# Performance work log

Measured on AMD Instinct MI355X. Metric: run time of the kernel, lower is better.

## Reference

```python
import jax, jax.numpy as jnp
import numpy as np

B = 256
IN_CH = 1
E = 8          # embedding_channels (power of 2)
DEPTH = 3      # log2(E)
T = 8192       # time_range
WINDOW = 2.0
K = 15         # kernel_size (odd -> torch 'same' == lax 'SAME')
TPI = 2.0 * np.pi


def conv1d(x, w, b, dilation=1, groups=1):
    # x: (B, Cin, T), w: (Cout, Cin/groups, K), b: (Cout,)
    out = jax.lax.conv_general_dilated(
        x, w, window_strides=(1,), padding='SAME',
        rhs_dilation=(dilation,),
        dimension_numbers=('NCH', 'OIH', 'NCH'),
        feature_group_count=groups)
    return out + b[None, :, None]


def setup_inputs() -> dict:
    key = jax.random.key(0)
    ks = jax.random.split(key, 14)
    s = 0.05
    x = jax.random.normal(ks[0], (B, T), jnp.float32)
    W1 = jax.random.normal(ks[1], (E, 2, 1, K), jnp.float32) * s   # per-channel Conv1d(1,2)
    b1 = jax.random.normal(ks[2], (E, 2), jnp.float32) * s
    W2 = jax.random.normal(ks[3], (E, 1, 2, K), jnp.float32) * s   # per-channel Conv1d(2,1)
    b2 = jax.random.normal(ks[4], (E, 1), jnp.float32) * s
    fcW = jax.random.normal(ks[5], (E, 2, T), jnp.float32) * 0.01  # per-channel Linear(T, 2)
    fcb = jax.random.normal(ks[6], (E, 2), jnp.float32) * s
    # deconv tree: level j has 2**(DEPTH-1-j) Conv1d(2,1) units, stacked as grouped conv
    dW0 = jax.random.normal(ks[7], (4, 2, K), jnp.float32) * s
    db0 = jax.random.normal(ks[8], (4,), jnp.float32) * s
    dW1 = jax.random.normal(ks[9], (2, 2, K), jnp.float32) * s
    db1 = jax.random.normal(ks[10], (2,), jnp.float32) * s
    dW2 = jax.random.normal(ks[11], (1, 2, K), jnp.float32) * s
    db2 = jax.random.normal(ks[12], (1,), jnp.float32) * s
    return dict(x=x, W1=W1, b1=b1, W2=W2, b2=b2, fcW=fcW, fcb=fcb,
                dW0=dW0, db0=db0, dW1=dW1, db1=db1, dW2=dW2, db2=db2)


def reference(x, W1, b1, W2, b2, fcW, fcb, dW0, db0, dW1, db1, dW2, db2):
    y = x.reshape(x.shape[0], IN_CH, T)
    # per-channel dilated conv stack (dilation = 2**i)
    chans = []
    for i in range(E):
        h = conv1d(y, W1[i], b1[i], dilation=2 ** i)
        chans.append(conv1d(h, W2[i], b2[i], dilation=2 ** i))
    latent = jnp.concatenate(chans, axis=1)                # (B, E, T)
    # FFT -> frequency / amplitude / offset
    rfft = jnp.fft.rfft(latent, axis=2)                    # (B, E, T//2+1)
    power = jnp.abs(rfft[:, :, 1:]) ** 2
    freqs = jnp.asarray(np.fft.rfftfreq(T)[1:] * T / WINDOW, jnp.float32)
    psum = jnp.sum(power, axis=2)
    f = jnp.sum(freqs * power, axis=2) / psum              # (B, E)
    a = 2.0 * jnp.sqrt(psum) / T
    b_off = rfft.real[:, :, 0] / T
    # per-channel Linear(T, 2) -> phase
    v = jnp.einsum('bet,ect->bec', latent, fcW) + fcb      # (B, E, 2)
    p = jnp.arctan2(v[..., 1], v[..., 0]) / TPI            # (B, E)
    # sinusoid reconstruction
    args = jnp.linspace(-WINDOW / 2, WINDOW / 2, T, dtype=jnp.float32)
    sig = a[..., None] * jnp.sin(TPI * (f[..., None] * args + p[..., None])) + b_off[..., None]
    # deconv tree: pairs of channels -> grouped conv, halving channels each level
    y = sig
    for dW, db in ((dW0, db0), (dW1, db1), (dW2, db2)):
        y = conv1d(y, dW, db, dilation=1, groups=dW.shape[0])
    out = y.reshape(y.shape[0], IN_CH * T)
    return (out, latent, sig,
            p[..., None], f[..., None], a[..., None], b_off[..., None])
```

## Files before the change

### kernel.cpp

```cpp
#include <hip/hip_runtime.h>
#include <math.h>

#define TT 8192
#define BB 256
#define EE 8
#define KK 15
#define PI_F  3.14159265358979323846f
#define TPI_F 6.28318530717958647692f

#define OFF_OUT 0
#define OFF_LAT (BB*TT)
#define OFF_SIG (OFF_LAT + BB*EE*TT)
#define OFF_P   (OFF_SIG + BB*EE*TT)
#define OFF_F   (OFF_P + BB*EE)
#define OFF_A   (OFF_F + BB*EE)
#define OFF_B0  (OFF_A + BB*EE)

#define SWZ(i) ((i) + ((i) >> 5))

__device__ __forceinline__ float rdfl(float v) {
  return __uint_as_float(__builtin_amdgcn_readfirstlane(__float_as_uint(v)));
}

__global__ __launch_bounds__(512) void conv_stack_kernel(
    const float* __restrict__ x, const float* __restrict__ W1,
    const float* __restrict__ b1, const float* __restrict__ W2,
    const float* __restrict__ b2, float* __restrict__ latent)
{
  extern __shared__ float smem[];
  const int h = blockIdx.x;
  const int e = blockIdx.y, b = blockIdx.z;
  const int d  = 1 << e;
  const int Mh = (TT/2) >> e;
  const int Lp = ((((Mh - 2) + 31) >> 5) << 5) + 30;
  float* sxp = smem;
  float* sW  = smem + d * Lp;
  const int tid = threadIdx.x;
  const float* xr = x + b * TT;
  const int tbase = h * (TT/2) - 14 * d;

  const int nstage = (TT/2) + 28 * d;
  for (int i = tid; i < nstage; i += 512) {
    int t  = tbase + i;
    int ph = i & (d - 1);
    int n  = i >> e;
    sxp[ph * Lp + n] = (t >= 0 && t < TT) ? xr[t] : 0.0f;
  }

  if (tid < 29) {
    float acc = 0.0f;
    for (int c = 0; c < 2; c++) {
      const float* w1 = W1 + e*30 + c*15;
      const float* w2 = W2 + e*30 + c*15;
      int jlo = tid - 14; if (jlo < 0) jlo = 0;
      int jhi = tid;      if (jhi > 14) jhi = 14;
      for (int j = jlo; j <= jhi; j++) acc += w2[j] * w1[tid - j];
    }
    sW[tid] = acc;
  } else if (tid == 29) {
    float s20 = 0.f, s21 = 0.f;
    for (int j = 0; j < 15; j++) { s20 += W2[e*30 + j]; s21 += W2[e*30 + 15 + j]; }
    sW[29] = b2[e] + s20*b1[e*2] + s21*b1[e*2 + 1];
  } else if (tid >= 32 && tid < 62) {
    sW[tid] = W1[e*30 + (tid - 32)];
  } else if (tid >= 64 && tid < 94) {
    sW[tid] = W2[e*30 + (tid - 64)];
  } else if (tid == 94 || tid == 95) {
    sW[tid] = b1[e*2 + (tid - 94)];
  }
  __syncthreads();

  float Wc[29];
  #pragma unroll
  for (int s = 0; s < 29; s++) Wc[s] = rdfl(sW[s]);
  const float Bc = rdfl(sW[29]);

  float* lr = latent + (b * EE + e) * TT + h * (TT/2);
  #pragma unroll 1
  for (int g = 0; g < 2; g++) {
    const int vt = g * 512 + tid;
    const int ph = vt & (d - 1);
    const int m0 = (vt >> e) << 2;

    float win[32];
    {
      const float2* wp = (const float2*)&sxp[ph * Lp + m0];
      #pragma unroll
      for (int v = 0; v < 16; v++) {
        float2 qv = wp[v];
        win[2*v] = qv.x; win[2*v+1] = qv.y;
      }
    }
    float acc[4] = {Bc, Bc, Bc, Bc};
    #pragma unroll
    for (int s = 0; s < 29; s++) {
      #pragma unroll
      for (int r = 0; r < 4; r++) acc[r] = fmaf(Wc[s], win[s + r], acc[r]);
    }

    if (h == 0 && g == 0 && m0 <= 6) {
      #pragma unroll
      for (int r = 0; r < 4; r++) {
        float corr = 0.0f;
        #pragma unroll
        for (int j = 0; j < 7; j++) {
          if (m0 + r + j <= 6) {
            float a0 = sW[94], a1 = sW[95];
            #pragma unroll
            for (int k = 0; k < 15; k++) {
              float xv = win[r + j + k];
              a0 = fmaf(sW[32 + k], xv, a0);
              a1 = fmaf(sW[47 + k], xv, a1);
            }
            corr = fmaf(sW[64 + j], a0, corr);
            corr = fmaf(sW[79 + j], a1, corr);
          }
        }
        acc[r] -= corr;
      }
    }
    if (h == 1 && g == 1 && m0 + 3 >= Mh - 7) {
      #pragma unroll
      for (int r = 0; r < 4; r++) {
        float corr = 0.0f;
        #pragma unroll
        for (int jj = 0; jj < 7; jj++) {
          const int j = 8 + jj;
          if (m0 + r + j >= Mh + 7) {
            float a0 = sW[94], a1 = sW[95];
            #pragma unroll
            for (int k = 0; k < 15; k++) {
              float xv = win[r + j + k];
              a0 = fmaf(sW[32 + k], xv, a0);
              a1 = fmaf(sW[47 + k], xv, a1);
            }
            corr = fmaf(sW[64 + j], a0, corr);
            corr = fmaf(sW[79 + j], a1, corr);
          }
        }
        acc[r] -= corr;
      }
    }

    #pragma unroll
    for (int r = 0; r < 4; r++) lr[ph + (m0 + r) * d] = acc[r];
  }
}

#define NF 4096

__device__ __forceinline__ int rev4(int k) {
  unsigned r = __brev((unsigned)k) >> 20;
  return (int)(((r & 0x555u) << 1) | ((r >> 1) & 0x555u));
}

__global__ __launch_bounds__(512) void fft_kernel(
    const float* __restrict__ latent, const float* __restrict__ fcW,
    const float* __restrict__ fcb, float* __restrict__ outP,
    float* __restrict__ outF, float* __restrict__ outA, float* __restrict__ outB0)
{
  __shared__ float re[SWZ(NF - 1) + 1];
  __shared__ float im[SWZ(NF - 1) + 1];
  __shared__ float rbuf[32];
  const int e = blockIdx.x, b = blockIdx.y, tid = threadIdx.x;
  const float2* row2 = (const float2*)(latent + (b*EE + e)*TT);
  const float2* f02  = (const float2*)(fcW + (e*2 + 0)*TT);
  const float2* f12  = (const float2*)(fcW + (e*2 + 1)*TT);

  float v0 = 0.f, v1 = 0.f;
  for (int n = tid; n < NF; n += 512) {
    float2 z = row2[n];
    re[SWZ(n)] = z.x; im[SWZ(n)] = z.y;
    float2 a0 = f02[n], a1 = f12[n];
    v0 = fmaf(z.x, a0.x, v0); v0 = fmaf(z.y, a0.y, v0);
    v1 = fmaf(z.x, a1.x, v1); v1 = fmaf(z.y, a1.y, v1);
  }
  __syncthreads();

  for (int L = NF >> 2; L >= 1; L >>= 2) {
    float wstep = -1.57079632679f / (float)L;
    for (int u = tid; u < (NF >> 2); u += 512) {
      int p = u & (L - 1);
      int base = ((u - p) << 2) + p;
      int i0 = SWZ(base), i1 = SWZ(base + L), i2 = SWZ(base + 2*L), i3 = SWZ(base + 3*L);
      float ar = re[i0], ai = im[i0];
      float br = re[i1], bi = im[i1];
      float cr = re[i2], ci = im[i2];
      float dr = re[i3], di = im[i3];
      float t0r = ar + cr, t0i = ai + ci;
      float t1r = ar - cr, t1i = ai - ci;
      float t2r = br + dr, t2i = bi + di;
      float t3r = br - dr, t3i = bi - di;
      float A0r = t0r + t2r, A0i = t0i + t2i;
      float A1r = t1r + t3i, A1i = t1i - t3r;
      float A2r = t0r - t2r, A2i = t0i - t2i;
      float A3r = t1r - t3i, A3i = t1i + t3r;
      float ang = wstep * (float)p;
      float s1 = __sinf(ang), c1 = __cosf(ang);
      float c2 = c1*c1 - s1*s1, s2 = 2.f*c1*s1;
      float c3 = c1*c2 - s1*s2, s3 = c1*s2 + s1*c2;
      re[i0] = A0r;                 im[i0] = A0i;
      re[i1] = A1r*c1 - A1i*s1;     im[i1] = A1r*s1 + A1i*c1;
      re[i2] = A2r*c2 - A2i*s2;     im[i2] = A2r*s2 + A2i*c2;
      re[i3] = A3r*c3 - A3i*s3;     im[i3] = A3r*s3 + A3i*c3;
    }
    __syncthreads();
  }

  float pacc = 0.f, facc = 0.f;
  for (int k = 1 + tid; k < NF; k += 512) {
    int jk = SWZ(rev4(k));
    int jm = SWZ(rev4(NF - k));
    float zr = re[jk], zi = im[jk];
    float yr = re[jm], yi = im[jm];
    float Er = 0.5f*(zr + yr), Ei = 0.5f*(zi - yi);
    float Dr = 0.5f*(zr - yr), Di = 0.5f*(zi + yi);
    float Or = Di, Oi = -Dr;
    float ang = -PI_F * (float)k / (float)NF;
    float s = __sinf(ang), c = __cosf(ang);
    float Xr = Er + c*Or - s*Oi;
    float Xi = Ei + c*Oi + s*Or;
    float mag = fmaf(Xr, Xr, Xi*Xi);
    pacc += mag;
    facc = fmaf(0.5f * (float)k, mag, facc);
  }
  if (tid == 0) {
    float X = re[SWZ(0)] - im[SWZ(0)];
    pacc += X*X;
    facc += 2048.0f * X*X;
  }

  #pragma unroll
  for (int off = 32; off > 0; off >>= 1) {
    pacc += __shfl_down(pacc, off);
    facc += __shfl_down(facc, off);
    v0   += __shfl_down(v0, off);
    v1   += __shfl_down(v1, off);
  }
  int wid = tid >> 6, lane = tid & 63;
  if (lane == 0) {
    rbuf[wid*4 + 0] = pacc; rbuf[wid*4 + 1] = facc;
    rbuf[wid*4 + 2] = v0;   rbuf[wid*4 + 3] = v1;
  }
  __syncthreads();
  if (tid == 0) {
    float P = 0.f, Fw = 0.f, V0 = 0.f, V1 = 0.f;
    #pragma unroll
    for (int w = 0; w < 8; w++) {
      P += rbuf[w*4]; Fw += rbuf[w*4+1]; V0 += rbuf[w*4+2]; V1 += rbuf[w*4+3];
    }
    float z0r = re[SWZ(0)], z0i = im[SWZ(0)];
    float amp  = 2.0f * sqrtf(P) / (float)TT;
    float boff = (z0r + z0i) / (float)TT;
    float vv0 = V0 + fcb[e*2 + 0];
    float vv1 = V1 + fcb[e*2 + 1];
    float ph  = atan2f(vv1, vv0) / TPI_F;
    int idx = b*EE + e;
    outP[idx]  = ph;
    outF[idx]  = Fw / P;
    outA[idx]  = amp;
    outB0[idx] = boff;
  }
}

#define TILE_C 512
#define SST 556
#define SL0 544
#define SL1 528

__global__ __launch_bounds__(256) void sig_deconv_kernel(
    const float* __restrict__ Pv, const float* __restrict__ Fv,
    const float* __restrict__ Av, const float* __restrict__ B0v,
    const float* __restrict__ dW0, const float* __restrict__ db0,
    const float* __restrict__ dW1, const float* __restrict__ db1,
    const float* __restrict__ dW2, const float* __restrict__ db2,
    float* __restrict__ sig, float* __restrict__ out)
{
  __shared__ float smem[4*SL0 + 8*SST];
  float* sl0  = smem;
  float* ssig = smem + 4*SL0;
  float* sl1  = smem + 4*SL0;

  const int tile = blockIdx.x, b = blockIdx.y;
  const int t0 = tile * TILE_C;
  const int tid = threadIdx.x;
  const float step = 2.0f / 8191.0f;

  float fs[8], am[8], psh[8], bo[8];
  #pragma unroll
  for (int ch = 0; ch < EE; ch++) {
    int idx = b*EE + ch;
    fs[ch] = Fv[idx]; am[ch] = Av[idx]; psh[ch] = Pv[idx]; bo[ch] = B0v[idx];
  }

  for (int i = tid; i < SST; i += 256) {
    int t = t0 + i - 21;
    bool in = (i < 554 && t >= 0 && t < TT);
    float arg = fmaf(step, (float)t, -1.0f);
    bool wr = (i >= 21 && i < 21 + TILE_C);
    #pragma unroll
    for (int ch = 0; ch < EE; ch++) {
      float rr = fmaf(fs[ch], arg, psh[ch]);
      rr -= rintf(rr);
      float val = in ? fmaf(am[ch], __sinf(TPI_F * rr), bo[ch]) : 0.0f;
      ssig[ch*SST + i] = val;
      if (wr) sig[(b*EE + ch)*TT + t] = val;
    }
  }
  __syncthreads();

  for (int g = 0; g < 4; g++) {
    float bg = db0[g];
    for (int u = tid; u < 135; u += 256) {
      const float4* p0 = (const float4*)(ssig + (2*g)*SST + 4*u);
      const float4* p1 = (const float4*)(ssig + (2*g+1)*SST + 4*u);
      float w0[20], w1[20];
      #pragma unroll
      for (int v = 0; v < 5; v++) {
        float4 q0 = p0[v], q1 = p1[v];
        w0[4*v]=q0.x; w0[4*v+1]=q0.y; w0[4*v+2]=q0.z; w0[4*v+3]=q0.w;
        w1[4*v]=q1.x; w1[4*v+1]=q1.y; w1[4*v+2]=q1.z; w1[4*v+3]=q1.w;
      }
      #pragma unroll
      for (int r = 0; r < 4; r++) {
        int i0 = 4*u + r;
        int t = t0 + i0 - 14;
        float a2 = bg;
        #pragma unroll
        for (int k = 0; k < KK; k++) {
          a2 = fmaf(dW0[g*30 + k],      w0[r + k], a2);
          a2 = fmaf(dW0[g*30 + 15 + k], w1[r + k], a2);
        }
        sl0[g*SL0 + i0] = (t >= 0 && t < TT) ? a2 : 0.0f;
      }
    }
  }
  if (tid < 16) sl0[(tid >> 2)*SL0 + 540 + (tid & 3)] = 0.0f;
  __syncthreads();

  for (int g = 0; g < 2; g++) {
    float bg = db1[g];
    for (int u = tid; u < 132; u += 256) {
      const float4* p0 = (const float4*)(sl0 + (2*g)*SL0 + 4*u);
      const float4* p1 = (const float4*)(sl0 + (2*g+1)*SL0 + 4*u);
      float w0[20], w1[20];
      #pragma unroll
      for (int v = 0; v < 5; v++) {
        float4 q0 = p0[v], q1 = p1[v];
        w0[4*v]=q0.x; w0[4*v+1]=q0.y; w0[4*v+2]=q0.z; w0[4*v+3]=q0.w;
        w1[4*v]=q1.x; w1[4*v+1]=q1.y; w1[4*v+2]=q1.z; w1[4*v+3]=q1.w;
      }
      #pragma unroll
      for (int r = 0; r < 4; r++) {
        int i1 = 4*u + r;
        if (i1 < 526) {
          int t = t0 + i1 - 7;
          float a2 = bg;
          #pragma unroll
          for (int k = 0; k < KK; k++) {
            a2 = fmaf(dW1[g*30 + k],      w0[r + k], a2);
            a2 = fmaf(dW1[g*30 + 15 + k], w1[r + k], a2);
          }
          sl1[g*SL1 + i1] = (t >= 0 && t < TT) ? a2 : 0.0f;
        }
      }
    }
  }
  __syncthreads();

  if (tid < 128) {
    float bg = db2[0];
    float* orow = out + b*TT + t0;
    int u = tid;
    const float4* p0 = (const float4*)(sl1 + 4*u);
    const float4* p1 = (const float4*)(sl1 + SL1 + 4*u);
    float w0[20], w1[20];
    #pragma unroll
    for (int v = 0; v < 5; v++) {
      float4 q0 = p0[v], q1 = p1[v];
      w0[4*v]=q0.x; w0[4*v+1]=q0.y; w0[4*v+2]=q0.z; w0[4*v+3]=q0.w;
      w1[4*v]=q1.x; w1[4*v+1]=q1.y; w1[4*v+2]=q1.z; w1[4*v+3]=q1.w;
    }
    float4 res;
    float* resf = (float*)&res;
    #pragma unroll
    for (int r = 0; r < 4; r++) {
      float a2 = bg;
      #pragma unroll
      for (int k = 0; k < KK; k++) {
        a2 = fmaf(dW2[k],      w0[r + k], a2);
        a2 = fmaf(dW2[15 + k], w1[r + k], a2);
      }
      resf[r] = a2;
    }
    ((float4*)orow)[u] = res;
  }
}

extern "C" void kernel_launch(void* const* d_in, const int* in_sizes, int n_in,
                              void* d_out, int out_size, void* d_ws, size_t ws_size,
                              hipStream_t stream) {
  const float* x   = (const float*)d_in[0];
  const float* W1  = (const float*)d_in[1];
  const float* b1  = (const float*)d_in[2];
  const float* W2  = (const float*)d_in[3];
  const float* b2  = (const float*)d_in[4];
  const float* fcW = (const float*)d_in[5];
  const float* fcb = (const float*)d_in[6];
  const float* dW0 = (const float*)d_in[7];
  const float* db0 = (const float*)d_in[8];
  const float* dW1 = (const float*)d_in[9];
  const float* db1 = (const float*)d_in[10];
  const float* dW2 = (const float*)d_in[11];
  const float* db2 = (const float*)d_in[12];

  float* o        = (float*)d_out;
  float* out_main = o + OFF_OUT;
  float* latent   = o + OFF_LAT;
  float* sig      = o + OFF_SIG;
  float* pP  = o + OFF_P;
  float* pF  = o + OFF_F;
  float* pA  = o + OFF_A;
  float* pB0 = o + OFF_B0;

  const size_t lds_conv = 8032 * sizeof(float);
  conv_stack_kernel<<<dim3(2, EE, BB), 512, lds_conv, stream>>>(x, W1, b1, W2, b2, latent);
  fft_kernel<<<dim3(EE, BB), 512, 0, stream>>>(latent, fcW, fcb, pP, pF, pA, pB0);
  sig_deconv_kernel<<<dim3(TT/TILE_C, BB), 256, 0, stream>>>(
      pP, pF, pA, pB0, dW0, db0, dW1, db1, dW2, db2, sig, out_main);
}
```

Baseline: 349.4 us.

## Fuse dilated conv stack into FFT kernel via shared-memory handoff

Merges the conv-stack and FFT kernels into one block per (batch, channel). The latent row is computed in two halves and written both to global memory and directly into the FFT's shared re/im arrays, so the FFT no longer re-reads latent from global memory. In exchange, LDS per block grows to about 66KB, which may lower occupancy. Grid parallelism also halves for the conv phase, since each block now processes both halves serially.

```diff
diff --git a/kernel.cpp b/kernel.cpp
--- a/kernel.cpp
+++ b/kernel.cpp
@@ -17,35 +17,45 @@
 #define OFF_B0  (OFF_A + BB*EE)
 
 #define SWZ(i) ((i) + ((i) >> 5))
+#define NF 4096
+
+#define L_RE   0
+#define L_IM   4223
+#define L_SXP  8446
+#define L_SW   16382
+#define L_RBUF 16478
+#define L_TOT  16510
 
 __device__ __forceinline__ float rdfl(float v) {
   return __uint_as_float(__builtin_amdgcn_readfirstlane(__float_as_uint(v)));
 }
 
-__global__ __launch_bounds__(512) void conv_stack_kernel(
+__device__ __forceinline__ int rev4(int k) {
+  unsigned r = __brev((unsigned)k) >> 20;
+  return (int)(((r & 0x555u) << 1) | ((r >> 1) & 0x555u));
+}
+
+__global__ __launch_bounds__(512) void conv_fft_kernel(
     const float* __restrict__ x, const float* __restrict__ W1,
     const float* __restrict__ b1, const float* __restrict__ W2,
-    const float* __restrict__ b2, float* __restrict__ latent)
+    const float* __restrict__ b2, const float* __restrict__ fcW,
+    const float* __restrict__ fcb, float* __restrict__ latent,
+    float* __restrict__ outP, float* __restrict__ outF,
+    float* __restrict__ outA, float* __restrict__ outB0)
 {
   extern __shared__ float smem[];
-  const int h = blockIdx.x;
-  const int e = blockIdx.y, b = blockIdx.z;
+  float* re   = smem + L_RE;
+  float* im   = smem + L_IM;
+  float* sxp  = smem + L_SXP;
+  float* sW   = smem + L_SW;
+  float* rbuf = smem + L_RBUF;
+
+  const int e = blockIdx.x, b = blockIdx.y;
   const int d  = 1 << e;
   const int Mh = (TT/2) >> e;
   const int Lp = ((((Mh - 2) + 31) >> 5) << 5) + 30;
-  float* sxp = smem;
-  float* sW  = smem + d * Lp;
   const int tid = threadIdx.x;
   const float* xr = x + b * TT;
-  const int tbase = h * (TT/2) - 14 * d;
-
-  const int nstage = (TT/2) + 28 * d;
-  for (int i = tid; i < nstage; i += 512) {
-    int t  = tbase + i;
-    int ph = i & (d - 1);
-    int n  = i >> e;
-    sxp[ph * Lp + n] = (t >= 0 && t < TT) ? xr[t] : 0.0f;
-  }
 
   if (tid < 29) {
     float acc = 0.0f;
@@ -68,112 +78,119 @@
   } else if (tid == 94 || tid == 95) {
     sW[tid] = b1[e*2 + (tid - 94)];
   }
-  __syncthreads();
 
   float Wc[29];
-  #pragma unroll
-  for (int s = 0; s < 29; s++) Wc[s] = rdfl(sW[s]);
-  const float Bc = rdfl(sW[29]);
-
-  float* lr = latent + (b * EE + e) * TT + h * (TT/2);
+  float Bc = 0.0f;
+  bool wloaded = false;
+
   #pragma unroll 1
-  for (int g = 0; g < 2; g++) {
-    const int vt = g * 512 + tid;
-    const int ph = vt & (d - 1);
-    const int m0 = (vt >> e) << 2;
-
-    float win[32];
-    {
-      const float2* wp = (const float2*)&sxp[ph * Lp + m0];
-      #pragma unroll
-      for (int v = 0; v < 16; v++) {
-        float2 qv = wp[v];
-        win[2*v] = qv.x; win[2*v+1] = qv.y;
-      }
-    }
-    float acc[4] = {Bc, Bc, Bc, Bc};
-    #pragma unroll
-    for (int s = 0; s < 29; s++) {
-      #pragma unroll
-      for (int r = 0; r < 4; r++) acc[r] = fmaf(Wc[s], win[s + r], acc[r]);
-    }
-
-    if (h == 0 && g == 0 && m0 <= 6) {
+  for (int h = 0; h < 2; ++h) {
+    const int tbase = h * (TT/2) - 14 * d;
+    const int nstage = (TT/2) + 28 * d;
+    for (int i = tid; i < nstage; i += 512) {
+      int t  = tbase + i;
+      int ph = i & (d - 1);
+      int n  = i >> e;
+      sxp[ph * Lp + n] = (t >= 0 && t < TT) ? xr[t] : 0.0f;
+    }
+    __syncthreads();
+
+    if (!wloaded) {
+      #pragma unroll
+      for (int s = 0; s < 29; s++) Wc[s] = rdfl(sW[s]);
+      Bc = rdfl(sW[29]);
+      wloaded = true;
+    }
+
+    float* lr = latent + (b * EE + e) * TT + h * (TT/2);
+
+    #pragma unroll 1
+    for (int g = 0; g < 2; g++) {
+      const int vt = g * 512 + tid;
+      const int ph = vt & (d - 1);
+      const int m0 = (vt >> e) << 2;
+
+      float win[32];
+      {
+        const float2* wp = (const float2*)&sxp[ph * Lp + m0];
+        #pragma unroll
+        for (int v = 0; v < 16; v++) {
+          float2 qv = wp[v];
+          win[2*v] = qv.x; win[2*v+1] = qv.y;
+        }
+      }
+      float acc[4] = {Bc, Bc, Bc, Bc};
+      #pragma unroll
+      for (int s = 0; s < 29; s++) {
+        #pragma unroll
+        for (int r = 0; r < 4; r++) acc[r] = fmaf(Wc[s], win[s + r], acc[r]);
+      }
+
+      if (h == 0 && g == 0 && m0 <= 6) {
+        #pragma unroll
+        for (int r = 0; r < 4; r++) {
+          float corr = 0.0f;
+          #pragma unroll
+          for (int j = 0; j < 7; j++) {
+            if (m0 + r + j <= 6) {
+              float a0 = sW[94], a1 = sW[95];
+              #pragma unroll
+              for (int k = 0; k < 15; k++) {
+                float xv = win[r + j + k];
+                a0 = fmaf(sW[32 + k], xv, a0);
+                a1 = fmaf(sW[47 + k], xv, a1);
+              }
+              corr = fmaf(sW[64 + j], a0, corr);
+              corr = fmaf(sW[79 + j], a1, corr);
+            }
+          }
+          acc[r] -= corr;
+        }
+      }
+      if (h == 1 && g == 1 && m0 + 3 >= Mh - 7) {
+        #pragma unroll
+        for (int r = 0; r < 4; r++) {
+          float corr = 0.0f;
+          #pragma unroll
+          for (int jj = 0; jj < 7; jj++) {
+            const int j = 8 + jj;
+            if (m0 + r + j >= Mh + 7) {
+              float a0 = sW[94], a1 = sW[95];
+              #pragma unroll
+              for (int k = 0; k < 15; k++) {
+                float xv = win[r + j + k];
+                a0 = fmaf(sW[32 + k], xv, a0);
+                a1 = fmaf(sW[47 + k], xv, a1);
+              }
+              corr = fmaf(sW[64 + j], a0, corr);
+              corr = fmaf(sW[79 + j], a1, corr);
+            }
+          }
+          acc[r] -= corr;
+        }
+      }
+
       #pragma unroll
       for (int r = 0; r < 4; r++) {
-        float corr = 0.0f;
-        #pragma unroll
-        for (int j = 0; j < 7; j++) {
-          if (m0 + r + j <= 6) {
-            float a0 = sW[94], a1 = sW[95];
-            #pragma unroll
-            for (int k = 0; k < 15; k++) {
-              float xv = win[r + j + k];
-              a0 = fmaf(sW[32 + k], xv, a0);
-              a1 = fmaf(sW[47 + k], xv, a1);
-            }
-            corr = fmaf(sW[64 + j], a0, corr);
-            corr = fmaf(sW[79 + j], a1, corr);
-          }
-        }
-        acc[r] -= corr;
-      }
-    }
-    if (h == 1 && g == 1 && m0 + 3 >= Mh - 7) {
-      #pragma unroll
-      for (int r = 0; r < 4; r++) {
-        float corr = 0.0f;
-        #pragma unroll
-        for (int jj = 0; jj < 7; jj++) {
-          const int j = 8 + jj;
-          if (m0 + r + j >= Mh + 7) {
-            float a0 = sW[94], a1 = sW[95];
-            #pragma unroll
-            for (int k = 0; k < 15; k++) {
-              float xv = win[r + j + k];
-              a0 = fmaf(sW[32 + k], xv, a0);
-              a1 = fmaf(sW[47 + k], xv, a1);
-            }
-            corr = fmaf(sW[64 + j], a0, corr);
-            corr = fmaf(sW[79 + j], a1, corr);
-          }
-        }
-        acc[r] -= corr;
-      }
-    }
-
-    #pragma unroll
-    for (int r = 0; r < 4; r++) lr[ph + (m0 + r) * d] = acc[r];
-  }
-}
-
-#define NF 4096
-
-__device__ __forceinline__ int rev4(int k) {
-  unsigned r = __brev((unsigned)k) >> 20;
-  return (int)(((r & 0x555u) << 1) | ((r >> 1) & 0x555u));
-}
-
-__global__ __launch_bounds__(512) void fft_kernel(
-    const float* __restrict__ latent, const float* __restrict__ fcW,
-    const float* __restrict__ fcb, float* __restrict__ outP,
-    float* __restrict__ outF, float* __restrict__ outA, float* __restrict__ outB0)
-{
-  __shared__ float re[SWZ(NF - 1) + 1];
-  __shared__ float im[SWZ(NF - 1) + 1];
-  __shared__ float rbuf[32];
-  const int e = blockIdx.x, b = blockIdx.y, tid = threadIdx.x;
-  const float2* row2 = (const float2*)(latent + (b*EE + e)*TT);
-  const float2* f02  = (const float2*)(fcW + (e*2 + 0)*TT);
-  const float2* f12  = (const float2*)(fcW + (e*2 + 1)*TT);
-
+        int toff = ph + (m0 + r) * d;
+        lr[toff] = acc[r];
+        int tg = h * (TT/2) + toff;
+        int n  = tg >> 1;
+        float* dst = (tg & 1) ? im : re;
+        dst[SWZ(n)] = acc[r];
+      }
+    }
+    __syncthreads();
+  }
+
+  const float2* f02 = (const float2*)(fcW + (e*2 + 0)*TT);
+  const float2* f12 = (const float2*)(fcW + (e*2 + 1)*TT);
   float v0 = 0.f, v1 = 0.f;
   for (int n = tid; n < NF; n += 512) {
-    float2 z = row2[n];
-    re[SWZ(n)] = z.x; im[SWZ(n)] = z.y;
+    float zr = re[SWZ(n)], zi = im[SWZ(n)];
     float2 a0 = f02[n], a1 = f12[n];
-    v0 = fmaf(z.x, a0.x, v0); v0 = fmaf(z.y, a0.y, v0);
-    v1 = fmaf(z.x, a1.x, v1); v1 = fmaf(z.y, a1.y, v1);
+    v0 = fmaf(zr, a0.x, v0); v0 = fmaf(zi, a0.y, v0);
+    v1 = fmaf(zr, a1.x, v1); v1 = fmaf(zi, a1.y, v1);
   }
   __syncthreads();
 
@@ -423,9 +440,9 @@
   float* pA  = o + OFF_A;
   float* pB0 = o + OFF_B0;
 
-  const size_t lds_conv = 8032 * sizeof(float);
-  conv_stack_kernel<<<dim3(2, EE, BB), 512, lds_conv, stream>>>(x, W1, b1, W2, b2, latent);
-  fft_kernel<<<dim3(EE, BB), 512, 0, stream>>>(latent, fcW, fcb, pP, pF, pA, pB0);
+  const size_t lds_fused = L_TOT * sizeof(float);
+  conv_fft_kernel<<<dim3(EE, BB), 512, lds_fused, stream>>>(
+      x, W1, b1, W2, b2, fcW, fcb, latent, pP, pF, pA, pB0);
   sig_deconv_kernel<<<dim3(TT/TILE_C, BB), 256, 0, stream>>>(
       pP, pF, pA, pB0, dW0, db0, dW1, db1, dW2, db2, sig, out_main);
 }
```

After: 343.7 us. No clear change (-1.6%).
